# Kernel tuning notes

Hardware: AMD Instinct MI355X
Metric: run time of the kernel (lower is better)

Reference implementation:

```python
import jax, jax.numpy as jnp
import numpy as np

B, S, V, D, H, DK, DH, L = 1, 2048, 256, 1024, 16, 64, 4096, 4
EPS = 1e-5
SCALE = 1.0 / np.sqrt(DK)


def _ln(x, g, b):
    mu = jnp.mean(x, axis=-1, keepdims=True)
    var = jnp.mean(jnp.square(x - mu), axis=-1, keepdims=True)
    return (x - mu) * jax.lax.rsqrt(var + EPS) * g + b


def setup_inputs() -> dict:
    key = jax.random.key(0)
    ks = jax.random.split(key, 20)
    f = lambda k, shape: (0.02 * jax.random.normal(k, shape)).astype(jnp.float32)
    return {
        "x": jax.random.randint(ks[0], (B, S), 0, V),
        "emb": f(ks[1], (V, D)),
        "pos": f(ks[2], (S, D)),
        "Wq": f(ks[3], (L, D, H * DK)), "bq": jnp.zeros((L, H * DK), jnp.float32),
        "Wk": f(ks[4], (L, D, H * DK)), "bk": jnp.zeros((L, H * DK), jnp.float32),
        "Wv": f(ks[5], (L, D, H * DK)), "bv": jnp.zeros((L, H * DK), jnp.float32),
        "Wo": f(ks[6], (L, H * DK, D)),
        "ln1_g": jnp.ones((L, D), jnp.float32), "ln1_b": jnp.zeros((L, D), jnp.float32),
        "W1": f(ks[7], (L, D, DH)), "b1": jnp.zeros((L, DH), jnp.float32),
        "W2": f(ks[8], (L, DH, D)), "b2": jnp.zeros((L, D), jnp.float32),
        "ln2_g": jnp.ones((L, D), jnp.float32), "ln2_b": jnp.zeros((L, D), jnp.float32),
        "head_w": f(ks[9], (D, V)), "head_b": jnp.zeros((V,), jnp.float32),
    }


def _forward(x, emb, pos, Wq, bq, Wk, bk, Wv, bv, Wo, ln1_g, ln1_b,
             W1, b1, W2, b2, ln2_g, ln2_b, head_w, head_b):
    h = emb[x] + pos[:S]                      # [B,S,D]
    causal = jnp.tril(jnp.ones((S, S), bool))  # additive -inf above diag
    for i in range(L):
        # --- naive attention: explicit QK^T, mask, softmax, @V ---
        q = (h @ Wq[i] + bq[i]).reshape(B, S, H, DK)
        k = (h @ Wk[i] + bk[i]).reshape(B, S, H, DK)
        v = (h @ Wv[i] + bv[i]).reshape(B, S, H, DK)
        scores = jnp.einsum('bqhd,bkhd->bhqk', q * SCALE, k)   # [B,H,S,S]
        scores = jnp.where(causal[None, None], scores, -jnp.inf)
        p = jax.nn.softmax(scores, axis=-1)
        a = jnp.einsum('bhqk,bkhd->bqhd', p, v).reshape(B, S, H * DK) @ Wo[i]
        # --- TransformerLayer: x + ln2(mlp(x + ln1(attn(x)))) ---
        u = h + _ln(a, ln1_g[i], ln1_b[i])
        m = jax.nn.gelu(u @ W1[i] + b1[i], approximate=False) @ W2[i] + b2[i]
        h = h + _ln(m, ln2_g[i], ln2_b[i])
    return h @ head_w + head_b                 # [B,S,V]


def reference(x, emb, pos, Wq, bq, Wk, bk, Wv, bv, Wo, ln1_g, ln1_b,
              W1, b1, W2, b2, ln2_g, ln2_b, head_w, head_b):
    return _forward(x, emb, pos, Wq, bq, Wk, bk, Wv, bv, Wo, ln1_g, ln1_b,
                    W1, b1, W2, b2, ln2_g, ln2_b, head_w, head_b)
```

## Files before the change

kernel.cpp:

```cpp
#include <hip/hip_runtime.h>
#include <hip/hip_bf16.h>
#include <cstdint>
#include <math.h>

static constexpr int S_  = 2048;
static constexpr int D_  = 1024;
static constexpr int H_  = 16;
static constexpr int DK_ = 64;
static constexpr int DH_ = 4096;
static constexpr int L_  = 4;
static constexpr int V_  = 256;
#define ATT_SCALE 0.125f

typedef __bf16 bf16;
typedef __bf16 bf16x8 __attribute__((ext_vector_type(8)));
typedef __bf16 bf16x4v __attribute__((ext_vector_type(4)));
typedef float  f32x4  __attribute__((ext_vector_type(4)));

__device__ __forceinline__ __attribute__((address_space(3))) void* to_lds(const void* p) {
  return (__attribute__((address_space(3))) void*)(uintptr_t)p;
}
__device__ __forceinline__ __attribute__((address_space(1))) void* to_glb(const void* p) {
  return (__attribute__((address_space(1))) void*)(uintptr_t)p;
}

template <int TN, int SPLIT, int GELU_EPI>
__device__ __forceinline__ void gemm_body(
    const bf16* __restrict__ A, const bf16* __restrict__ Bt,
    const float* __restrict__ bias, float* __restrict__ Cf, bf16* __restrict__ Cb,
    float* __restrict__ P0, float* __restrict__ P1,
    int M, int N, int K)
{
  constexpr int BU = TN / 32;
  constexpr int JN = TN / 32;
  __shared__ __align__(16) bf16 sA[2][128 * 64];
  __shared__ __align__(16) bf16 sB[2][TN * 64];
  const int tid  = threadIdx.x;
  const int wave = tid >> 6;
  const int lane = tid & 63;
  const int l16  = lane & 15;
  const int quad = lane >> 4;
  const int bm = blockIdx.x * 128;
  const int bn = blockIdx.y * TN;
  const int wm = (wave & 1) * 64;
  const int wn = (wave >> 1) * (TN / 2);

  const int KS = K / SPLIT;
  const size_t kofs = (SPLIT > 1) ? (size_t)blockIdx.z * KS : 0;

  const int srow = tid >> 3;
  const int sc8  = (tid & 7) ^ (srow & 7);
  const bf16* gA = A  + (size_t)(bm + srow) * K + kofs + sc8 * 8;
  const bf16* gB = Bt + (size_t)(bn + srow) * K + kofs + sc8 * 8;

  const int swz = l16 & 7;

  f32x4 acc[4][JN] = {};

#pragma unroll
  for (int u = 0; u < 4; ++u)
    __builtin_amdgcn_global_load_lds(to_glb(gA + (size_t)u * 32 * K),
                                     to_lds(&sA[0][u * 2048 + tid * 8]), 16, 0, 0);
#pragma unroll
  for (int u = 0; u < BU; ++u)
    __builtin_amdgcn_global_load_lds(to_glb(gB + (size_t)u * 32 * K),
                                     to_lds(&sB[0][u * 2048 + tid * 8]), 16, 0, 0);

  int cur = 0;
  for (int k0 = 0; k0 < KS; k0 += 64, cur ^= 1) {
    if (k0 + 64 < KS) {
      const int nb = cur ^ 1;
      const size_t ko = k0 + 64;
#pragma unroll
      for (int u = 0; u < 4; ++u)
        __builtin_amdgcn_global_load_lds(to_glb(gA + ko + (size_t)u * 32 * K),
                                         to_lds(&sA[nb][u * 2048 + tid * 8]), 16, 0, 0);
#pragma unroll
      for (int u = 0; u < BU; ++u)
        __builtin_amdgcn_global_load_lds(to_glb(gB + ko + (size_t)u * 32 * K),
                                         to_lds(&sB[nb][u * 2048 + tid * 8]), 16, 0, 0);
      if constexpr (BU == 4) asm volatile("s_waitcnt vmcnt(8)" ::: "memory");
      else                   asm volatile("s_waitcnt vmcnt(6)" ::: "memory");
    } else {
      asm volatile("s_waitcnt vmcnt(0)" ::: "memory");
    }
    __builtin_amdgcn_s_barrier();

    bf16x8 af[2][4], bfv[2][JN];
#pragma unroll
    for (int kc = 0; kc < 2; ++kc) {
      const int c8 = ((kc * 4 + quad) ^ swz) * 8;
#pragma unroll
      for (int i = 0; i < 4; ++i)
        af[kc][i] = *(const bf16x8*)&sA[cur][(wm + i * 16 + l16) * 64 + c8];
#pragma unroll
      for (int j = 0; j < JN; ++j)
        bfv[kc][j] = *(const bf16x8*)&sB[cur][(wn + j * 16 + l16) * 64 + c8];
    }
    asm volatile("s_waitcnt lgkmcnt(0)" ::: "memory");
    __builtin_amdgcn_s_barrier();

#pragma unroll
    for (int kc = 0; kc < 2; ++kc)
#pragma unroll
      for (int i = 0; i < 4; ++i)
#pragma unroll
        for (int j = 0; j < JN; ++j)
          acc[i][j] = __builtin_amdgcn_mfma_f32_16x16x32_bf16(af[kc][i], bfv[kc][j], acc[i][j], 0, 0, 0);
  }

  if constexpr (SPLIT > 1) {
    float* Pf;
    if constexpr (SPLIT == 4)
      Pf = (blockIdx.z < 2) ? (P0 + (size_t)blockIdx.z * ((size_t)M * N))
                            : (P1 + (size_t)(blockIdx.z - 2) * ((size_t)M * N));
    else
      Pf = P0 + (size_t)blockIdx.z * ((size_t)M * N);
#pragma unroll
    for (int i = 0; i < 4; ++i)
#pragma unroll
      for (int j = 0; j < JN; ++j) {
        const int col = bn + wn + j * 16 + l16;
#pragma unroll
        for (int r = 0; r < 4; ++r) {
          const int row = bm + wm + i * 16 + quad * 4 + r;
          Pf[(size_t)row * N + col] = acc[i][j][r];
        }
      }
  } else {
#pragma unroll
    for (int i = 0; i < 4; ++i) {
#pragma unroll
      for (int j = 0; j < JN; ++j) {
        const int col = bn + wn + j * 16 + l16;
        const float bz = bias ? bias[col] : 0.0f;
#pragma unroll
        for (int r = 0; r < 4; ++r) {
          const int row = bm + wm + i * 16 + quad * 4 + r;
          float v = acc[i][j][r] + bz;
          if (GELU_EPI) v = 0.5f * v * (1.0f + erff(v * 0.70710678118654752f));
          if (Cf) Cf[(size_t)row * N + col] = v;
          if (Cb) Cb[(size_t)row * N + col] = (bf16)v;
        }
      }
    }
  }
}

__global__ __launch_bounds__(256) void gemm_qkv_kernel(
    const bf16* __restrict__ A, const bf16* __restrict__ Bt,
    const float* __restrict__ bias, bf16* __restrict__ Cb, int M, int N, int K)
{ gemm_body<64, 1, 0>(A, Bt, bias, nullptr, Cb, nullptr, nullptr, M, N, K); }

__global__ __launch_bounds__(256) void gemm_wo_kernel(
    const bf16* __restrict__ A, const bf16* __restrict__ Bt,
    float* __restrict__ P0, int M, int N, int K)
{ gemm_body<128, 2, 0>(A, Bt, nullptr, nullptr, nullptr, P0, nullptr, M, N, K); }

__global__ __launch_bounds__(256) void gemm_mlp1_kernel(
    const bf16* __restrict__ A, const bf16* __restrict__ Bt,
    const float* __restrict__ bias, bf16* __restrict__ Cb, int M, int N, int K)
{ gemm_body<128, 1, 1>(A, Bt, bias, nullptr, Cb, nullptr, nullptr, M, N, K); }

__global__ __launch_bounds__(256) void gemm_mlp2_kernel(
    const bf16* __restrict__ A, const bf16* __restrict__ Bt,
    float* __restrict__ P0, float* __restrict__ P1, int M, int N, int K)
{ gemm_body<128, 4, 0>(A, Bt, nullptr, nullptr, nullptr, P0, P1, M, N, K); }

__global__ __launch_bounds__(256) void gemm_head_kernel(
    const bf16* __restrict__ A, const bf16* __restrict__ Bt,
    float* __restrict__ P0, float* __restrict__ P1, int M, int N, int K)
{ gemm_body<64, 4, 0>(A, Bt, nullptr, nullptr, nullptr, P0, P1, M, N, K); }

template <int SPLIT>
__device__ __forceinline__ void splitk_reduce_body(
    const float* __restrict__ P0, const float* __restrict__ P1,
    const float* __restrict__ bias, float* __restrict__ Cf,
    size_t MN, int N)
{
  const size_t i = ((size_t)blockIdx.x * 256 + threadIdx.x) * 4;
  const float4 a = *(const float4*)(P0 + i);
  const float4 b = *(const float4*)(P0 + MN + i);
  float4 o;
  o.x = a.x + b.x; o.y = a.y + b.y; o.z = a.z + b.z; o.w = a.w + b.w;
  if constexpr (SPLIT == 4) {
    const float4 c = *(const float4*)(P1 + i);
    const float4 d = *(const float4*)(P1 + MN + i);
    o.x += c.x + d.x; o.y += c.y + d.y; o.z += c.z + d.z; o.w += c.w + d.w;
  }
  if (bias) {
    const int col = (int)(i & (size_t)(N - 1));
    const float4 bz = *(const float4*)(bias + col);
    o.x += bz.x; o.y += bz.y; o.z += bz.z; o.w += bz.w;
  }
  *(float4*)(Cf + i) = o;
}

__global__ __launch_bounds__(256) void splitk_reduce2_kernel(
    const float* __restrict__ P0, const float* __restrict__ bias,
    float* __restrict__ Cf, size_t MN, int N)
{ splitk_reduce_body<2>(P0, nullptr, bias, Cf, MN, N); }

__global__ __launch_bounds__(256) void splitk_reduce4_kernel(
    const float* __restrict__ P0, const float* __restrict__ P1,
    const float* __restrict__ bias, float* __restrict__ Cf, size_t MN, int N)
{ splitk_reduce_body<4>(P0, P1, bias, Cf, MN, N); }

__global__ __launch_bounds__(256) void transpose_cast_kernel(
    const float* __restrict__ in, bf16* __restrict__ out, int K, int N)
{
  __shared__ float t[32][33];
  const int k0 = blockIdx.y * 32;
  const int n0 = blockIdx.x * 32;
  const int tx = threadIdx.x & 31;
  const int ty = threadIdx.x >> 5;
#pragma unroll
  for (int i = 0; i < 32; i += 8)
    t[ty + i][tx] = in[(size_t)(k0 + ty + i) * N + (n0 + tx)];
  __syncthreads();
#pragma unroll
  for (int i = 0; i < 32; i += 8)
    out[(size_t)(n0 + ty + i) * K + (k0 + tx)] = (bf16)t[tx][ty + i];
}

__global__ __launch_bounds__(256) void transpose3_cast_kernel(
    const float* __restrict__ in0, const float* __restrict__ in1, const float* __restrict__ in2,
    bf16* __restrict__ out, int K, int N)
{
  const float* in = (blockIdx.z == 0) ? in0 : (blockIdx.z == 1) ? in1 : in2;
  bf16* o = out + (size_t)blockIdx.z * K * N;
  __shared__ float t[32][33];
  const int k0 = blockIdx.y * 32;
  const int n0 = blockIdx.x * 32;
  const int tx = threadIdx.x & 31;
  const int ty = threadIdx.x >> 5;
#pragma unroll
  for (int i = 0; i < 32; i += 8)
    t[ty + i][tx] = in[(size_t)(k0 + ty + i) * N + (n0 + tx)];
  __syncthreads();
#pragma unroll
  for (int i = 0; i < 32; i += 8)
    o[(size_t)(n0 + ty + i) * K + (k0 + tx)] = (bf16)t[tx][ty + i];
}

__global__ __launch_bounds__(256) void vtrans_kernel(
    const bf16* __restrict__ qkv, bf16* __restrict__ vT)
{
  __shared__ bf16 t[32][65];
  const int s0 = blockIdx.x * 32;
  const int head = blockIdx.y;
  const int sr = threadIdx.x >> 3, d8 = (threadIdx.x & 7) * 8;
  bf16x8 v = *(const bf16x8*)(qkv + (size_t)(s0 + sr) * (3 * D_) + 2 * D_ + head * DK_ + d8);
#pragma unroll
  for (int i = 0; i < 8; ++i) t[sr][d8 + i] = v[i];
  __syncthreads();
  const int dw = threadIdx.x >> 2, s4 = (threadIdx.x & 3) * 8;
  bf16x8 o;
#pragma unroll
  for (int i = 0; i < 8; ++i) o[i] = t[s4 + i][dw];
  *(bf16x8*)(vT + (size_t)head * DK_ * S_ + (size_t)dw * S_ + s0 + s4) = o;
}

__global__ __launch_bounds__(256) void embed_kernel(
    const int* __restrict__ x, const float* __restrict__ emb, const float* __restrict__ pos,
    float* __restrict__ hf, bf16* __restrict__ hb)
{
  const int s = blockIdx.x;
  const int d = threadIdx.x * 4;
  const int tok = x[s];
  const float4 e = *(const float4*)(emb + (size_t)tok * D_ + d);
  const float4 p = *(const float4*)(pos + (size_t)s * D_ + d);
  float4 o; o.x = e.x + p.x; o.y = e.y + p.y; o.z = e.z + p.z; o.w = e.w + p.w;
  *(float4*)(hf + (size_t)s * D_ + d) = o;
  bf16x4v ob = {(bf16)o.x, (bf16)o.y, (bf16)o.z, (bf16)o.w};
  *(bf16x4v*)(hb + (size_t)s * D_ + d) = ob;
}

__device__ __forceinline__ float wave_reduce_sum(float v) {
#pragma unroll
  for (int off = 32; off > 0; off >>= 1) v += __shfl_xor(v, off, 64);
  return v;
}

__global__ __launch_bounds__(256) void ln_add_kernel(
    const float* __restrict__ src, const float* __restrict__ resid,
    const float* __restrict__ g, const float* __restrict__ b,
    float* __restrict__ outf, bf16* __restrict__ outb)
{
  const int r = blockIdx.x;
  const int t = threadIdx.x;
  const float4 x = ((const float4*)(src + (size_t)r * D_))[t];
  float s  = x.x + x.y + x.z + x.w;
  float s2 = x.x * x.x + x.y * x.y + x.z * x.z + x.w * x.w;
  s  = wave_reduce_sum(s);
  s2 = wave_reduce_sum(s2);
  __shared__ float red[8];
  const int wave = t >> 6, lane = t & 63;
  if (lane == 0) { red[wave] = s; red[4 + wave] = s2; }
  __syncthreads();
  s  = red[0] + red[1] + red[2] + red[3];
  s2 = red[4] + red[5] + red[6] + red[7];
  const float mu  = s * (1.0f / 1024.0f);
  const float var = s2 * (1.0f / 1024.0f) - mu * mu;
  const float rs  = rsqrtf(var + 1e-5f);
  const float4 gv = ((const float4*)g)[t];
  const float4 bv = ((const float4*)b)[t];
  const float4 hv = ((const float4*)(resid + (size_t)r * D_))[t];
  const float o0 = hv.x + (x.x - mu) * rs * gv.x + bv.x;
  const float o1 = hv.y + (x.y - mu) * rs * gv.y + bv.y;
  const float o2 = hv.z + (x.z - mu) * rs * gv.z + bv.z;
  const float o3 = hv.w + (x.w - mu) * rs * gv.w + bv.w;
  if (outf) { float4 o4; o4.x = o0; o4.y = o1; o4.z = o2; o4.w = o3;
              ((float4*)(outf + (size_t)r * D_))[t] = o4; }
  if (outb) { bf16x4v ob = {(bf16)o0, (bf16)o1, (bf16)o2, (bf16)o3};
              ((bf16x4v*)(outb + (size_t)r * D_))[t] = ob; }
}

__global__ __launch_bounds__(256) void attn_mfma_kernel(
    const bf16* __restrict__ qkv, const bf16* __restrict__ vT, bf16* __restrict__ out)
{
  __shared__ __align__(16) bf16 sK[2][64 * 64];
  __shared__ __align__(16) bf16 sV[2][64 * 64];
  __shared__ __align__(16) bf16 sP[4][16 * 64];

  const int head = blockIdx.y;
  const int xb   = blockIdx.x;
  const int qIdx = (head & 8) ? (31 - xb) : xb;
  const int qb   = qIdx * 64;
  const int tid  = threadIdx.x;
  const int wave = tid >> 6, lane = tid & 63;
  const int l16  = lane & 15, quad = lane >> 4;
  const int swz  = l16 & 7;

  const size_t rstr = 3 * D_;
  const bf16* kbase = qkv + D_ + head * DK_;
  const bf16* vbase = vT + (size_t)head * DK_ * S_;

  const int srow   = tid >> 3;
  const int kchunk = (tid & 7) ^ (srow & 7);

  bf16x8 aq0, aq1;
  {
    const bf16* qrow = qkv + (size_t)(qb + wave * 16 + l16) * rstr + head * DK_ + quad * 8;
    bf16x8 t0 = *(const bf16x8*)(qrow);
    bf16x8 t1 = *(const bf16x8*)(qrow + 32);
#pragma unroll
    for (int i = 0; i < 8; ++i) {
      aq0[i] = (bf16)((float)t0[i] * ATT_SCALE);
      aq1[i] = (bf16)((float)t1[i] * ATT_SCALE);
    }
  }

  f32x4 oa[4] = {};
  float lsum[4] = {0.0f, 0.0f, 0.0f, 0.0f};
  const int qrow0 = qb + wave * 16 + quad * 4;
  const int jmax = qb + 63;

#pragma unroll
  for (int u = 0; u < 2; ++u) {
    const int r = u * 32 + srow;
    __builtin_amdgcn_global_load_lds(to_glb(kbase + (size_t)r * rstr + kchunk * 8),
                                     to_lds(&sK[0][u * 2048 + tid * 8]), 16, 0, 0);
    __builtin_amdgcn_global_load_lds(to_glb(vbase + (size_t)r * S_ + kchunk * 8),
                                     to_lds(&sV[0][u * 2048 + tid * 8]), 16, 0, 0);
  }

  int cur = 0;
  for (int j0 = 0; j0 <= jmax; j0 += 64, cur ^= 1) {
    if (j0 + 64 <= jmax) {
      const int nb = cur ^ 1;
      const int jn = j0 + 64;
#pragma unroll
      for (int u = 0; u < 2; ++u) {
        const int r = u * 32 + srow;
        __builtin_amdgcn_global_load_lds(to_glb(kbase + (size_t)(jn + r) * rstr + kchunk * 8),
                                         to_lds(&sK[nb][u * 2048 + tid * 8]), 16, 0, 0);
        __builtin_amdgcn_global_load_lds(to_glb(vbase + (size_t)r * S_ + jn + kchunk * 8),
                                         to_lds(&sV[nb][u * 2048 + tid * 8]), 16, 0, 0);
      }
      asm volatile("s_waitcnt vmcnt(4)" ::: "memory");
    } else {
      asm volatile("s_waitcnt vmcnt(0)" ::: "memory");
    }
    __builtin_amdgcn_s_barrier();

    f32x4 sc[4];
#pragma unroll
    for (int n = 0; n < 4; ++n) {
      const bf16* kr = &sK[cur][(n * 16 + l16) * 64];
      bf16x8 bk0 = *(const bf16x8*)(kr + ((quad    ) ^ swz) * 8);
      bf16x8 bk1 = *(const bf16x8*)(kr + ((quad + 4) ^ swz) * 8);
      f32x4 z = {};
      z = __builtin_amdgcn_mfma_f32_16x16x32_bf16(aq0, bk0, z, 0, 0, 0);
      z = __builtin_amdgcn_mfma_f32_16x16x32_bf16(aq1, bk1, z, 0, 0, 0);
      sc[n] = z;
    }
    bf16 pb[4][4];
#pragma unroll
    for (int n = 0; n < 4; ++n) {
      const int key = j0 + n * 16 + l16;
#pragma unroll
      for (int r = 0; r < 4; ++r) {
        const float p = (key <= qrow0 + r) ? __expf(sc[n][r]) : 0.0f;
        lsum[r] += p;
        pb[n][r] = (bf16)p;
      }
    }
    bf16* pw = &sP[wave][0];
    const int cb = l16 >> 3, co = l16 & 7;
#pragma unroll
    for (int n = 0; n < 4; ++n) {
#pragma unroll
      for (int r = 0; r < 4; ++r) {
        const int row = quad * 4 + r;
        const int ch = (2 * n + cb) ^ (row & 7);
        pw[row * 64 + ch * 8 + co] = pb[n][r];
      }
    }
    asm volatile("s_waitcnt lgkmcnt(0)" ::: "memory");
    __builtin_amdgcn_wave_barrier();
    bf16x8 ap0 = *(const bf16x8*)&pw[l16 * 64 + ((quad    ) ^ swz) * 8];
    bf16x8 ap1 = *(const bf16x8*)&pw[l16 * 64 + ((quad + 4) ^ swz) * 8];

#pragma unroll
    for (int n = 0; n < 4; ++n) {
      const bf16* vr = &sV[cur][(n * 16 + l16) * 64];
      bf16x8 bv0 = *(const bf16x8*)(vr + ((quad    ) ^ swz) * 8);
      bf16x8 bv1 = *(const bf16x8*)(vr + ((quad + 4) ^ swz) * 8);
      oa[n] = __builtin_amdgcn_mfma_f32_16x16x32_bf16(ap0, bv0, oa[n], 0, 0, 0);
      oa[n] = __builtin_amdgcn_mfma_f32_16x16x32_bf16(ap1, bv1, oa[n], 0, 0, 0);
    }
    asm volatile("s_waitcnt lgkmcnt(0)" ::: "memory");
    __builtin_amdgcn_s_barrier();
  }

#pragma unroll
  for (int r = 0; r < 4; ++r) {
#pragma unroll
    for (int off = 1; off <= 8; off <<= 1)
      lsum[r] += __shfl_xor(lsum[r], off, 64);
  }
#pragma unroll
  for (int r = 0; r < 4; ++r) {
    const float inv = 1.0f / lsum[r];
    const int qrow = qrow0 + r;
#pragma unroll
    for (int n = 0; n < 4; ++n)
      out[(size_t)qrow * D_ + head * DK_ + n * 16 + l16] = (bf16)(oa[n][r] * inv);
  }
}

__global__ __launch_bounds__(256) void pack3_kernel(
    const float* __restrict__ a, const float* __restrict__ b, const float* __restrict__ c,
    float* __restrict__ out)
{
  const int i = blockIdx.x * 256 + threadIdx.x;
  if (i < 1024) out[i] = a[i];
  else if (i < 2048) out[i] = b[i - 1024];
  else if (i < 3072) out[i] = c[i - 2048];
}

extern "C" void kernel_launch(void* const* d_in, const int* in_sizes, int n_in,
                              void* d_out, int out_size, void* d_ws, size_t ws_size,
                              hipStream_t stream)
{
  const int*   x     = (const int*)d_in[0];
  const float* emb   = (const float*)d_in[1];
  const float* pos   = (const float*)d_in[2];
  const float* Wq    = (const float*)d_in[3];
  const float* bq    = (const float*)d_in[4];
  const float* Wk    = (const float*)d_in[5];
  const float* bk    = (const float*)d_in[6];
  const float* Wv    = (const float*)d_in[7];
  const float* bv    = (const float*)d_in[8];
  const float* Wo    = (const float*)d_in[9];
  const float* ln1g  = (const float*)d_in[10];
  const float* ln1b  = (const float*)d_in[11];
  const float* W1    = (const float*)d_in[12];
  const float* b1    = (const float*)d_in[13];
  const float* W2    = (const float*)d_in[14];
  const float* b2    = (const float*)d_in[15];
  const float* ln2g  = (const float*)d_in[16];
  const float* ln2b  = (const float*)d_in[17];
  const float* headw = (const float*)d_in[18];
  const float* headb = (const float*)d_in[19];

  char* w = (char*)d_ws;
  float* h_f32   = (float*)w;  w += (size_t)S_ * D_ * 4;
  bf16*  h_b     = (bf16*)w;   w += (size_t)S_ * D_ * 2;
  bf16*  qkv_b   = (bf16*)w;   w += (size_t)S_ * 3 * D_ * 2;
  bf16*  attn_b  = (bf16*)w;   w += (size_t)S_ * D_ * 2;
  float* a_f32   = (float*)w;  w += (size_t)S_ * D_ * 4;
  bf16*  u_b     = (bf16*)w;   w += (size_t)S_ * D_ * 2;
  bf16*  mh_b    = (bf16*)w;   w += (size_t)S_ * DH_ * 2;
  float* m_f32   = (float*)w;  w += (size_t)S_ * D_ * 4;
  bf16*  qkvT    = (bf16*)w;   w += (size_t)3 * D_ * D_ * 2;
  bf16*  woT     = (bf16*)w;   w += (size_t)D_ * D_ * 2;
  bf16*  w1T     = (bf16*)w;   w += (size_t)DH_ * D_ * 2;
  bf16*  w2T     = (bf16*)w;   w += (size_t)D_ * DH_ * 2;
  bf16*  headT   = (bf16*)w;   w += (size_t)V_ * D_ * 2;
  float* qkvbias = (float*)w;  w += (size_t)3 * D_ * 4;
  bf16*  vT      = qkvT;

  float* woP  = (float*)u_b;
  float* m2P0 = (float*)attn_b;
  float* m2P1 = (float*)qkvT;
  float* hP0  = (float*)attn_b;
  float* hP1  = hP0 + 2 * (size_t)S_ * V_;

  embed_kernel<<<dim3(S_), dim3(256), 0, stream>>>(x, emb, pos, h_f32, h_b);
  transpose_cast_kernel<<<dim3(V_ / 32, D_ / 32), dim3(256), 0, stream>>>(headw, headT, D_, V_);

  for (int i = 0; i < L_; ++i) {
    const float* Wq_i = Wq + (size_t)i * D_ * D_;
    const float* Wk_i = Wk + (size_t)i * D_ * D_;
    const float* Wv_i = Wv + (size_t)i * D_ * D_;
    const float* Wo_i = Wo + (size_t)i * D_ * D_;
    const float* W1_i = W1 + (size_t)i * D_ * DH_;
    const float* W2_i = W2 + (size_t)i * DH_ * D_;

    transpose3_cast_kernel<<<dim3(D_ / 32, D_ / 32, 3), dim3(256), 0, stream>>>(
        Wq_i, Wk_i, Wv_i, qkvT, D_, D_);
    pack3_kernel<<<dim3(12), dim3(256), 0, stream>>>(bq + (size_t)i * D_, bk + (size_t)i * D_, bv + (size_t)i * D_, qkvbias);
    gemm_qkv_kernel<<<dim3(S_ / 128, 3 * D_ / 64), dim3(256), 0, stream>>>(
        h_b, qkvT, qkvbias, qkv_b, S_, 3 * D_, D_);
    vtrans_kernel<<<dim3(S_ / 32, H_), dim3(256), 0, stream>>>(qkv_b, vT);
    attn_mfma_kernel<<<dim3(S_ / 64, H_), dim3(256), 0, stream>>>(qkv_b, vT, attn_b);
    transpose_cast_kernel<<<dim3(D_ / 32, D_ / 32), dim3(256), 0, stream>>>(Wo_i, woT, D_, D_);
    gemm_wo_kernel<<<dim3(S_ / 128, D_ / 128, 2), dim3(256), 0, stream>>>(
        attn_b, woT, woP, S_, D_, D_);
    splitk_reduce2_kernel<<<dim3((unsigned)((size_t)S_ * D_ / 1024)), dim3(256), 0, stream>>>(
        woP, nullptr, a_f32, (size_t)S_ * D_, D_);
    ln_add_kernel<<<dim3(S_), dim3(256), 0, stream>>>(
        a_f32, h_f32, ln1g + (size_t)i * D_, ln1b + (size_t)i * D_, nullptr, u_b);
    transpose_cast_kernel<<<dim3(DH_ / 32, D_ / 32), dim3(256), 0, stream>>>(W1_i, w1T, D_, DH_);
    gemm_mlp1_kernel<<<dim3(S_ / 128, DH_ / 128), dim3(256), 0, stream>>>(
        u_b, w1T, b1 + (size_t)i * DH_, mh_b, S_, DH_, D_);
    transpose_cast_kernel<<<dim3(D_ / 32, DH_ / 32), dim3(256), 0, stream>>>(W2_i, w2T, DH_, D_);
    gemm_mlp2_kernel<<<dim3(S_ / 128, D_ / 128, 4), dim3(256), 0, stream>>>(
        mh_b, w2T, m2P0, m2P1, S_, D_, DH_);
    splitk_reduce4_kernel<<<dim3((unsigned)((size_t)S_ * D_ / 1024)), dim3(256), 0, stream>>>(
        m2P0, m2P1, b2 + (size_t)i * D_, m_f32, (size_t)S_ * D_, D_);
    ln_add_kernel<<<dim3(S_), dim3(256), 0, stream>>>(
        m_f32, h_f32, ln2g + (size_t)i * D_, ln2b + (size_t)i * D_, h_f32, h_b);
  }

  gemm_head_kernel<<<dim3(S_ / 128, V_ / 64, 4), dim3(256), 0, stream>>>(
      h_b, headT, hP0, hP1, S_, V_, D_);
  splitk_reduce4_kernel<<<dim3((unsigned)((size_t)S_ * V_ / 1024)), dim3(256), 0, stream>>>(
      hP0, hP1, headb, (float*)d_out, (size_t)S_ * V_, V_);
}
```

Measured before the change: 868.0 us.

## Fuse split-K reductions into LayerNorm, swizzle GEMM tiles, hoist bias packing

The separate split-K reduce kernels before each LayerNorm are removed, and the LayerNorm kernels now sum the split-K partials (plus bias) themselves. This saves one full fp32 activation write and re-read per reduction. The GEMM block index is remapped with an XCD-style swizzle to improve L2 locality across chiplets. The MLP1 tile width is narrowed to 64, and the per-layer QKV bias packing is hoisted into a single launch. The swizzle hardcodes 16 M-tiles and assumes the grid size is divisible by 8, which ties it to these shapes.

Result: faster. 850.9 us (-2.0%).

```diff
diff --git a/kernel.cpp b/kernel.cpp
--- a/kernel.cpp
+++ b/kernel.cpp
@@ -40,8 +40,13 @@
   const int lane = tid & 63;
   const int l16  = lane & 15;
   const int quad = lane >> 4;
-  const int bm = blockIdx.x * 128;
-  const int bn = blockIdx.y * TN;
+
+  const int idl = blockIdx.y * 16 + blockIdx.x;
+  const int qch = (gridDim.x * gridDim.y) >> 3;
+  const int wsw = (idl & 7) * qch + (idl >> 3);
+  const int bm  = (wsw & 15) * 128;
+  const int bn  = (wsw >> 4) * TN;
+
   const int wm = (wave & 1) * 64;
   const int wn = (wave >> 1) * (TN / 2);
 
@@ -115,7 +120,7 @@
       Pf = (blockIdx.z < 2) ? (P0 + (size_t)blockIdx.z * ((size_t)M * N))
                             : (P1 + (size_t)(blockIdx.z - 2) * ((size_t)M * N));
     else
-      Pf = P0 + (size_t)blockIdx.z * ((size_t)M * N);
+      Pf = (blockIdx.z == 0) ? P0 : P1;
 #pragma unroll
     for (int i = 0; i < 4; ++i)
 #pragma unroll
@@ -154,13 +159,13 @@
 
 __global__ __launch_bounds__(256) void gemm_wo_kernel(
     const bf16* __restrict__ A, const bf16* __restrict__ Bt,
-    float* __restrict__ P0, int M, int N, int K)
-{ gemm_body<128, 2, 0>(A, Bt, nullptr, nullptr, nullptr, P0, nullptr, M, N, K); }
+    float* __restrict__ P0, float* __restrict__ P1, int M, int N, int K)
+{ gemm_body<128, 2, 0>(A, Bt, nullptr, nullptr, nullptr, P0, P1, M, N, K); }
 
 __global__ __launch_bounds__(256) void gemm_mlp1_kernel(
     const bf16* __restrict__ A, const bf16* __restrict__ Bt,
     const float* __restrict__ bias, bf16* __restrict__ Cb, int M, int N, int K)
-{ gemm_body<128, 1, 1>(A, Bt, bias, nullptr, Cb, nullptr, nullptr, M, N, K); }
+{ gemm_body<64, 1, 1>(A, Bt, bias, nullptr, Cb, nullptr, nullptr, M, N, K); }
 
 __global__ __launch_bounds__(256) void gemm_mlp2_kernel(
     const bf16* __restrict__ A, const bf16* __restrict__ Bt,
@@ -172,108 +177,22 @@
     float* __restrict__ P0, float* __restrict__ P1, int M, int N, int K)
 { gemm_body<64, 4, 0>(A, Bt, nullptr, nullptr, nullptr, P0, P1, M, N, K); }
 
-template <int SPLIT>
-__device__ __forceinline__ void splitk_reduce_body(
+__global__ __launch_bounds__(256) void splitk_reduce4_kernel(
     const float* __restrict__ P0, const float* __restrict__ P1,
-    const float* __restrict__ bias, float* __restrict__ Cf,
-    size_t MN, int N)
+    const float* __restrict__ bias, float* __restrict__ Cf, size_t MN, int N)
 {
   const size_t i = ((size_t)blockIdx.x * 256 + threadIdx.x) * 4;
   const float4 a = *(const float4*)(P0 + i);
   const float4 b = *(const float4*)(P0 + MN + i);
+  const float4 c = *(const float4*)(P1 + i);
+  const float4 d = *(const float4*)(P1 + MN + i);
   float4 o;
-  o.x = a.x + b.x; o.y = a.y + b.y; o.z = a.z + b.z; o.w = a.w + b.w;
-  if constexpr (SPLIT == 4) {
-    const float4 c = *(const float4*)(P1 + i);
-    const float4 d = *(const float4*)(P1 + MN + i);
-    o.x += c.x + d.x; o.y += c.y + d.y; o.z += c.z + d.z; o.w += c.w + d.w;
-  }
-  if (bias) {
-    const int col = (int)(i & (size_t)(N - 1));
-    const float4 bz = *(const float4*)(bias + col);
-    o.x += bz.x; o.y += bz.y; o.z += bz.z; o.w += bz.w;
-  }
+  o.x = a.x + b.x + c.x + d.x; o.y = a.y + b.y + c.y + d.y;
+  o.z = a.z + b.z + c.z + d.z; o.w = a.w + b.w + c.w + d.w;
+  const int col = (int)(i & (size_t)(N - 1));
+  const float4 bz = *(const float4*)(bias + col);
+  o.x += bz.x; o.y += bz.y; o.z += bz.z; o.w += bz.w;
   *(float4*)(Cf + i) = o;
-}
-
-__global__ __launch_bounds__(256) void splitk_reduce2_kernel(
-    const float* __restrict__ P0, const float* __restrict__ bias,
-    float* __restrict__ Cf, size_t MN, int N)
-{ splitk_reduce_body<2>(P0, nullptr, bias, Cf, MN, N); }
-
-__global__ __launch_bounds__(256) void splitk_reduce4_kernel(
-    const float* __restrict__ P0, const float* __restrict__ P1,
-    const float* __restrict__ bias, float* __restrict__ Cf, size_t MN, int N)
-{ splitk_reduce_body<4>(P0, P1, bias, Cf, MN, N); }
-
-__global__ __launch_bounds__(256) void transpose_cast_kernel(
-    const float* __restrict__ in, bf16* __restrict__ out, int K, int N)
-{
-  __shared__ float t[32][33];
-  const int k0 = blockIdx.y * 32;
-  const int n0 = blockIdx.x * 32;
-  const int tx = threadIdx.x & 31;
-  const int ty = threadIdx.x >> 5;
-#pragma unroll
-  for (int i = 0; i < 32; i += 8)
-    t[ty + i][tx] = in[(size_t)(k0 + ty + i) * N + (n0 + tx)];
-  __syncthreads();
-#pragma unroll
-  for (int i = 0; i < 32; i += 8)
-    out[(size_t)(n0 + ty + i) * K + (k0 + tx)] = (bf16)t[tx][ty + i];
-}
-
-__global__ __launch_bounds__(256) void transpose3_cast_kernel(
-    const float* __restrict__ in0, const float* __restrict__ in1, const float* __restrict__ in2,
-    bf16* __restrict__ out, int K, int N)
-{
-  const float* in = (blockIdx.z == 0) ? in0 : (blockIdx.z == 1) ? in1 : in2;
-  bf16* o = out + (size_t)blockIdx.z * K * N;
-  __shared__ float t[32][33];
-  const int k0 = blockIdx.y * 32;
-  const int n0 = blockIdx.x * 32;
-  const int tx = threadIdx.x & 31;
-  const int ty = threadIdx.x >> 5;
-#pragma unroll
-  for (int i = 0; i < 32; i += 8)
-    t[ty + i][tx] = in[(size_t)(k0 + ty + i) * N + (n0 + tx)];
-  __syncthreads();
-#pragma unroll
-  for (int i = 0; i < 32; i += 8)
-    o[(size_t)(n0 + ty + i) * K + (k0 + tx)] = (bf16)t[tx][ty + i];
-}
-
-__global__ __launch_bounds__(256) void vtrans_kernel(
-    const bf16* __restrict__ qkv, bf16* __restrict__ vT)
-{
-  __shared__ bf16 t[32][65];
-  const int s0 = blockIdx.x * 32;
-  const int head = blockIdx.y;
-  const int sr = threadIdx.x >> 3, d8 = (threadIdx.x & 7) * 8;
-  bf16x8 v = *(const bf16x8*)(qkv + (size_t)(s0 + sr) * (3 * D_) + 2 * D_ + head * DK_ + d8);
-#pragma unroll
-  for (int i = 0; i < 8; ++i) t[sr][d8 + i] = v[i];
-  __syncthreads();
-  const int dw = threadIdx.x >> 2, s4 = (threadIdx.x & 3) * 8;
-  bf16x8 o;
-#pragma unroll
-  for (int i = 0; i < 8; ++i) o[i] = t[s4 + i][dw];
-  *(bf16x8*)(vT + (size_t)head * DK_ * S_ + (size_t)dw * S_ + s0 + s4) = o;
-}
-
-__global__ __launch_bounds__(256) void embed_kernel(
-    const int* __restrict__ x, const float* __restrict__ emb, const float* __restrict__ pos,
-    float* __restrict__ hf, bf16* __restrict__ hb)
-{
-  const int s = blockIdx.x;
-  const int d = threadIdx.x * 4;
-  const int tok = x[s];
-  const float4 e = *(const float4*)(emb + (size_t)tok * D_ + d);
-  const float4 p = *(const float4*)(pos + (size_t)s * D_ + d);
-  float4 o; o.x = e.x + p.x; o.y = e.y + p.y; o.z = e.z + p.z; o.w = e.w + p.w;
-  *(float4*)(hf + (size_t)s * D_ + d) = o;
-  bf16x4v ob = {(bf16)o.x, (bf16)o.y, (bf16)o.z, (bf16)o.w};
-  *(bf16x4v*)(hb + (size_t)s * D_ + d) = ob;
 }
 
 __device__ __forceinline__ float wave_reduce_sum(float v) {
@@ -282,14 +201,33 @@
   return v;
 }
 
-__global__ __launch_bounds__(256) void ln_add_kernel(
-    const float* __restrict__ src, const float* __restrict__ resid,
+template <int SPLIT>
+__device__ __forceinline__ void ln_fused_body(
+    const float* __restrict__ P0, const float* __restrict__ P1,
+    const float* __restrict__ bias, const float* __restrict__ resid,
     const float* __restrict__ g, const float* __restrict__ b,
-    float* __restrict__ outf, bf16* __restrict__ outb)
+    float* __restrict__ outf, bf16* __restrict__ outb, size_t MN)
 {
   const int r = blockIdx.x;
   const int t = threadIdx.x;
-  const float4 x = ((const float4*)(src + (size_t)r * D_))[t];
+  const size_t ro = (size_t)r * D_;
+  float4 x;
+  {
+    const float4 a0 = ((const float4*)(P0 + ro))[t];
+    float4 a1;
+    if constexpr (SPLIT == 2) a1 = ((const float4*)(P1 + ro))[t];
+    else                      a1 = ((const float4*)(P0 + MN + ro))[t];
+    x.x = a0.x + a1.x; x.y = a0.y + a1.y; x.z = a0.z + a1.z; x.w = a0.w + a1.w;
+    if constexpr (SPLIT == 4) {
+      const float4 a2 = ((const float4*)(P1 + ro))[t];
+      const float4 a3 = ((const float4*)(P1 + MN + ro))[t];
+      x.x += a2.x + a3.x; x.y += a2.y + a3.y; x.z += a2.z + a3.z; x.w += a2.w + a3.w;
+    }
+  }
+  if (bias) {
+    const float4 bz = ((const float4*)bias)[t];
+    x.x += bz.x; x.y += bz.y; x.z += bz.z; x.w += bz.w;
+  }
   float s  = x.x + x.y + x.z + x.w;
   float s2 = x.x * x.x + x.y * x.y + x.z * x.z + x.w * x.w;
   s  = wave_reduce_sum(s);
@@ -305,15 +243,98 @@
   const float rs  = rsqrtf(var + 1e-5f);
   const float4 gv = ((const float4*)g)[t];
   const float4 bv = ((const float4*)b)[t];
-  const float4 hv = ((const float4*)(resid + (size_t)r * D_))[t];
+  const float4 hv = ((const float4*)(resid + ro))[t];
   const float o0 = hv.x + (x.x - mu) * rs * gv.x + bv.x;
   const float o1 = hv.y + (x.y - mu) * rs * gv.y + bv.y;
   const float o2 = hv.z + (x.z - mu) * rs * gv.z + bv.z;
   const float o3 = hv.w + (x.w - mu) * rs * gv.w + bv.w;
   if (outf) { float4 o4; o4.x = o0; o4.y = o1; o4.z = o2; o4.w = o3;
-              ((float4*)(outf + (size_t)r * D_))[t] = o4; }
+              ((float4*)(outf + ro))[t] = o4; }
   if (outb) { bf16x4v ob = {(bf16)o0, (bf16)o1, (bf16)o2, (bf16)o3};
-              ((bf16x4v*)(outb + (size_t)r * D_))[t] = ob; }
+              ((bf16x4v*)(outb + ro))[t] = ob; }
+}
+
+__global__ __launch_bounds__(256) void ln_fused2_kernel(
+    const float* __restrict__ P0, const float* __restrict__ P1,
+    const float* __restrict__ resid, const float* __restrict__ g,
+    const float* __restrict__ b, bf16* __restrict__ outb, size_t MN)
+{ ln_fused_body<2>(P0, P1, nullptr, resid, g, b, nullptr, outb, MN); }
+
+__global__ __launch_bounds__(256) void ln_fused4_kernel(
+    const float* __restrict__ P0, const float* __restrict__ P1,
+    const float* __restrict__ bias, const float* __restrict__ resid,
+    const float* __restrict__ g, const float* __restrict__ b,
+    float* __restrict__ outf, bf16* __restrict__ outb, size_t MN)
+{ ln_fused_body<4>(P0, P1, bias, resid, g, b, outf, outb, MN); }
+
+__global__ __launch_bounds__(256) void transpose_cast_kernel(
+    const float* __restrict__ in, bf16* __restrict__ out, int K, int N)
+{
+  __shared__ float t[32][33];
+  const int k0 = blockIdx.y * 32;
+  const int n0 = blockIdx.x * 32;
+  const int tx = threadIdx.x & 31;
+  const int ty = threadIdx.x >> 5;
+#pragma unroll
+  for (int i = 0; i < 32; i += 8)
+    t[ty + i][tx] = in[(size_t)(k0 + ty + i) * N + (n0 + tx)];
+  __syncthreads();
+#pragma unroll
+  for (int i = 0; i < 32; i += 8)
+    out[(size_t)(n0 + ty + i) * K + (k0 + tx)] = (bf16)t[tx][ty + i];
+}
+
+__global__ __launch_bounds__(256) void transpose3_cast_kernel(
+    const float* __restrict__ in0, const float* __restrict__ in1, const float* __restrict__ in2,
+    bf16* __restrict__ out, int K, int N)
+{
+  const float* in = (blockIdx.z == 0) ? in0 : (blockIdx.z == 1) ? in1 : in2;
+  bf16* o = out + (size_t)blockIdx.z * K * N;
+  __shared__ float t[32][33];
+  const int k0 = blockIdx.y * 32;
+  const int n0 = blockIdx.x * 32;
+  const int tx = threadIdx.x & 31;
+  const int ty = threadIdx.x >> 5;
+#pragma unroll
+  for (int i = 0; i < 32; i += 8)
+    t[ty + i][tx] = in[(size_t)(k0 + ty + i) * N + (n0 + tx)];
+  __syncthreads();
+#pragma unroll
+  for (int i = 0; i < 32; i += 8)
+    o[(size_t)(n0 + ty + i) * K + (k0 + tx)] = (bf16)t[tx][ty + i];
+}
+
+__global__ __launch_bounds__(256) void vtrans_kernel(
+    const bf16* __restrict__ qkv, bf16* __restrict__ vT)
+{
+  __shared__ bf16 t[32][65];
+  const int s0 = blockIdx.x * 32;
+  const int head = blockIdx.y;
+  const int sr = threadIdx.x >> 3, d8 = (threadIdx.x & 7) * 8;
+  bf16x8 v = *(const bf16x8*)(qkv + (size_t)(s0 + sr) * (3 * D_) + 2 * D_ + head * DK_ + d8);
+#pragma unroll
+  for (int i = 0; i < 8; ++i) t[sr][d8 + i] = v[i];
+  __syncthreads();
+  const int dw = threadIdx.x >> 2, s4 = (threadIdx.x & 3) * 8;
+  bf16x8 o;
+#pragma unroll
+  for (int i = 0; i < 8; ++i) o[i] = t[s4 + i][dw];
+  *(bf16x8*)(vT + (size_t)head * DK_ * S_ + (size_t)dw * S_ + s0 + s4) = o;
+}
+
+__global__ __launch_bounds__(256) void embed_kernel(
+    const int* __restrict__ x, const float* __restrict__ emb, const float* __restrict__ pos,
+    float* __restrict__ hf, bf16* __restrict__ hb)
+{
+  const int s = blockIdx.x;
+  const int d = threadIdx.x * 4;
+  const int tok = x[s];
+  const float4 e = *(const float4*)(emb + (size_t)tok * D_ + d);
+  const float4 p = *(const float4*)(pos + (size_t)s * D_ + d);
+  float4 o; o.x = e.x + p.x; o.y = e.y + p.y; o.z = e.z + p.z; o.w = e.w + p.w;
+  *(float4*)(hf + (size_t)s * D_ + d) = o;
+  bf16x4v ob = {(bf16)o.x, (bf16)o.y, (bf16)o.z, (bf16)o.w};
+  *(bf16x4v*)(hb + (size_t)s * D_ + d) = ob;
 }
 
 __global__ __launch_bounds__(256) void attn_mfma_kernel(
@@ -450,14 +471,17 @@
   }
 }
 
-__global__ __launch_bounds__(256) void pack3_kernel(
+__global__ __launch_bounds__(256) void pack3_all_kernel(
     const float* __restrict__ a, const float* __restrict__ b, const float* __restrict__ c,
     float* __restrict__ out)
 {
   const int i = blockIdx.x * 256 + threadIdx.x;
-  if (i < 1024) out[i] = a[i];
-  else if (i < 2048) out[i] = b[i - 1024];
-  else if (i < 3072) out[i] = c[i - 2048];
+  const int l = blockIdx.y;
+  float v;
+  if (i < 1024) v = a[l * 1024 + i];
+  else if (i < 2048) v = b[l * 1024 + i - 1024];
+  else v = c[l * 1024 + i - 2048];
+  out[(size_t)l * 3072 + i] = v;
 }
 
 extern "C" void kernel_launch(void* const* d_in, const int* in_sizes, int n_in,
@@ -499,17 +523,19 @@
   bf16*  w1T     = (bf16*)w;   w += (size_t)DH_ * D_ * 2;
   bf16*  w2T     = (bf16*)w;   w += (size_t)D_ * DH_ * 2;
   bf16*  headT   = (bf16*)w;   w += (size_t)V_ * D_ * 2;
-  float* qkvbias = (float*)w;  w += (size_t)3 * D_ * 4;
+  float* qkvbias = (float*)w;  w += (size_t)L_ * 3 * D_ * 4;
   bf16*  vT      = qkvT;
 
-  float* woP  = (float*)u_b;
+  float* woP0 = a_f32;
+  float* woP1 = m_f32;
   float* m2P0 = (float*)attn_b;
   float* m2P1 = (float*)qkvT;
   float* hP0  = (float*)attn_b;
-  float* hP1  = hP0 + 2 * (size_t)S_ * V_;
+  float* hP1  = (float*)a_f32;
 
   embed_kernel<<<dim3(S_), dim3(256), 0, stream>>>(x, emb, pos, h_f32, h_b);
   transpose_cast_kernel<<<dim3(V_ / 32, D_ / 32), dim3(256), 0, stream>>>(headw, headT, D_, V_);
+  pack3_all_kernel<<<dim3(12, L_), dim3(256), 0, stream>>>(bq, bk, bv, qkvbias);
 
   for (int i = 0; i < L_; ++i) {
     const float* Wq_i = Wq + (size_t)i * D_ * D_;
@@ -521,28 +547,24 @@
 
     transpose3_cast_kernel<<<dim3(D_ / 32, D_ / 32, 3), dim3(256), 0, stream>>>(
         Wq_i, Wk_i, Wv_i, qkvT, D_, D_);
-    pack3_kernel<<<dim3(12), dim3(256), 0, stream>>>(bq + (size_t)i * D_, bk + (size_t)i * D_, bv + (size_t)i * D_, qkvbias);
     gemm_qkv_kernel<<<dim3(S_ / 128, 3 * D_ / 64), dim3(256), 0, stream>>>(
-        h_b, qkvT, qkvbias, qkv_b, S_, 3 * D_, D_);
+        h_b, qkvT, qkvbias + (size_t)i * 3 * D_, qkv_b, S_, 3 * D_, D_);
     vtrans_kernel<<<dim3(S_ / 32, H_), dim3(256), 0, stream>>>(qkv_b, vT);
     attn_mfma_kernel<<<dim3(S_ / 64, H_), dim3(256), 0, stream>>>(qkv_b, vT, attn_b);
     transpose_cast_kernel<<<dim3(D_ / 32, D_ / 32), dim3(256), 0, stream>>>(Wo_i, woT, D_, D_);
     gemm_wo_kernel<<<dim3(S_ / 128, D_ / 128, 2), dim3(256), 0, stream>>>(
-        attn_b, woT, woP, S_, D_, D_);
-    splitk_reduce2_kernel<<<dim3((unsigned)((size_t)S_ * D_ / 1024)), dim3(256), 0, stream>>>(
-        woP, nullptr, a_f32, (size_t)S_ * D_, D_);
-    ln_add_kernel<<<dim3(S_), dim3(256), 0, stream>>>(
-        a_f32, h_f32, ln1g + (size_t)i * D_, ln1b + (size_t)i * D_, nullptr, u_b);
+        attn_b, woT, woP0, woP1, S_, D_, D_);
+    ln_fused2_kernel<<<dim3(S_), dim3(256), 0, stream>>>(
+        woP0, woP1, h_f32, ln1g + (size_t)i * D_, ln1b + (size_t)i * D_, u_b, (size_t)S_ * D_);
     transpose_cast_kernel<<<dim3(DH_ / 32, D_ / 32), dim3(256), 0, stream>>>(W1_i, w1T, D_, DH_);
-    gemm_mlp1_kernel<<<dim3(S_ / 128, DH_ / 128), dim3(256), 0, stream>>>(
+    gemm_mlp1_kernel<<<dim3(S_ / 128, DH_ / 64), dim3(256), 0, stream>>>(
         u_b, w1T, b1 + (size_t)i * DH_, mh_b, S_, DH_, D_);
     transpose_cast_kernel<<<dim3(D_ / 32, DH_ / 32), dim3(256), 0, stream>>>(W2_i, w2T, DH_, D_);
     gemm_mlp2_kernel<<<dim3(S_ / 128, D_ / 128, 4), dim3(256), 0, stream>>>(
         mh_b, w2T, m2P0, m2P1, S_, D_, DH_);
-    splitk_reduce4_kernel<<<dim3((unsigned)((size_t)S_ * D_ / 1024)), dim3(256), 0, stream>>>(
-        m2P0, m2P1, b2 + (size_t)i * D_, m_f32, (size_t)S_ * D_, D_);
-    ln_add_kernel<<<dim3(S_), dim3(256), 0, stream>>>(
-        m_f32, h_f32, ln2g + (size_t)i * D_, ln2b + (size_t)i * D_, h_f32, h_b);
+    ln_fused4_kernel<<<dim3(S_), dim3(256), 0, stream>>>(
+        m2P0, m2P1, b2 + (size_t)i * D_, h_f32, ln2g + (size_t)i * D_, ln2b + (size_t)i * D_,
+        h_f32, h_b, (size_t)S_ * D_);
   }
 
   gemm_head_kernel<<<dim3(S_ / 128, V_ / 64, 4), dim3(256), 0, stream>>>(
```
